# Kernel tuning notes

Measured on AMD Instinct MI355X. Metric: run time of the kernel, lower is better.

Reference implementation:

```python
import jax, jax.numpy as jnp
import numpy as np

EPS = 1e-5

def layer_norm(x, gamma):
    mu = jnp.mean(x, axis=-1, keepdims=True)
    var = jnp.mean(jnp.square(x - mu), axis=-1, keepdims=True)
    return (x - mu) / jnp.sqrt(var + EPS) * gamma

def setup_inputs() -> dict:
    key = jax.random.key(0)
    ks = jax.random.split(key, 10)
    b, n, j = 2, 2048, 2048
    dim, ctx_dim, heads, dim_head, ff_mult = 1024, 1024, 16, 64, 4
    inner = heads * dim_head
    ff_inner = ff_mult * dim
    s = 0.02
    return {
        'x': jax.random.normal(ks[0], (b, n, dim), jnp.float32),
        'context': jax.random.normal(ks[1], (b, j, ctx_dim), jnp.float32),
        'mask': jax.random.randint(ks[2], (b, j), 0, 2, jnp.int32),
        'gamma': jnp.ones((dim,), jnp.float32),
        'ctx_gamma': jnp.ones((ctx_dim,), jnp.float32),
        'Wq': jax.random.normal(ks[3], (dim, inner), jnp.float32) * s,
        'Wkv': jax.random.normal(ks[4], (ctx_dim, 2 * dim_head), jnp.float32) * s,
        'Wout': jax.random.normal(ks[5], (inner, dim), jnp.float32) * s,
        'Wff1': jax.random.normal(ks[6], (dim, 2 * ff_inner), jnp.float32) * s,
        'Wff2': jax.random.normal(ks[7], (ff_inner, dim), jnp.float32) * s,
    }

def reference(x, context, mask, gamma, ctx_gamma, Wq, Wkv, Wout, Wff1, Wff2):
    heads, dim_head = 16, 64
    b, n, dim = x.shape
    scale = dim_head ** -0.5
    xn = layer_norm(x, gamma)                              # [b,n,dim]
    ctx = layer_norm(context, ctx_gamma)                   # [b,j,cd]
    q = (xn @ Wq).reshape(b, n, heads, dim_head).transpose(0, 2, 1, 3) * scale  # [b,h,n,d]
    kv = ctx @ Wkv                                         # [b,j,2d]
    k, v = kv[..., :dim_head], kv[..., dim_head:]          # [b,j,d] each (multi-query)
    sim = jnp.einsum('bhid,bjd->bhij', q, k)               # [b,h,n,j]
    sim = jnp.where((mask == 0)[:, None, None, :], -jnp.inf, sim)
    attn = jax.nn.softmax(sim, axis=-1)
    out = jnp.einsum('bhij,bjd->bhid', attn, v)            # [b,h,n,d]
    out = out.transpose(0, 2, 1, 3).reshape(b, n, heads * dim_head)
    out = out @ Wout                                       # [b,n,dim]
    # parallel SwiGLU FF on normalized x
    h = xn @ Wff1
    ff_inner = Wff2.shape[0]
    a, gate = h[..., :ff_inner], h[..., ff_inner:]
    out = out + (jax.nn.silu(gate) * a) @ Wff2
    return out
```

## Files before the change

### kernel.cpp

```cpp
#include <hip/hip_runtime.h>

typedef unsigned short u16;
typedef unsigned int   u32;
typedef __bf16  bf16x8 __attribute__((ext_vector_type(8)));
typedef __bf16  bf16x2 __attribute__((ext_vector_type(2)));
typedef u16     u16x8  __attribute__((ext_vector_type(8)));
typedef float   f32x4  __attribute__((ext_vector_type(4)));

static __device__ __forceinline__ float b2f(u16 v) {
    return __builtin_bit_cast(float, (u32)(((u32)v) << 16));
}
static __device__ __forceinline__ u16 f2b(float f) {
    u32 u = __builtin_bit_cast(u32, f);
    return (u16)((u + 0x7FFFu + ((u >> 16) & 1u)) >> 16);
}
static __device__ __forceinline__ u32 pack2(float a, float b) {
    bf16x2 t; t[0] = (__bf16)a; t[1] = (__bf16)b;
    return __builtin_bit_cast(u32, t);
}

__global__ __launch_bounds__(256)
void ln_kernel(const float* __restrict__ x, const float* __restrict__ ctx,
               const float* __restrict__ gamma, const float* __restrict__ cgamma,
               u16* __restrict__ xn, u16* __restrict__ ctxn)
{
    const int row = blockIdx.x;
    const int tid = threadIdx.x;
    const float* src; const float* g; u16* dst;
    if (row < 4096) { src = x   + (long)row * 1024;          g = gamma;  dst = xn   + (long)row * 1024; }
    else            { src = ctx + (long)(row - 4096) * 1024; g = cgamma; dst = ctxn + (long)(row - 4096) * 1024; }
    float4 v = ((const float4*)src)[tid];
    float s = v.x + v.y + v.z + v.w;
    float q = v.x*v.x + v.y*v.y + v.z*v.z + v.w*v.w;
#pragma unroll
    for (int off = 32; off; off >>= 1) { s += __shfl_xor(s, off); q += __shfl_xor(q, off); }
    __shared__ float r1[4], r2[4];
    if ((tid & 63) == 0) { r1[tid >> 6] = s; r2[tid >> 6] = q; }
    __syncthreads();
    s = r1[0] + r1[1] + r1[2] + r1[3];
    q = r2[0] + r2[1] + r2[2] + r2[3];
    float mu   = s * (1.0f / 1024.0f);
    float var  = q * (1.0f / 1024.0f) - mu * mu;
    float rstd = rsqrtf(var + 1e-5f);
    float4 gv = ((const float4*)g)[tid];
    ushort4 o;
    o.x = f2b((v.x - mu) * rstd * gv.x);
    o.y = f2b((v.y - mu) * rstd * gv.y);
    o.z = f2b((v.z - mu) * rstd * gv.z);
    o.w = f2b((v.w - mu) * rstd * gv.w);
    ((ushort4*)dst)[tid] = o;
}

__global__ __launch_bounds__(256)
void wconv(const float* __restrict__ W, u16* __restrict__ Wt, int N, int K, float scale)
{
    __shared__ float tile[32][33];
    const int tid = threadIdx.x;
    const int n0 = blockIdx.x * 32;
    const int k0 = blockIdx.y * 32;
    const int r  = tid >> 3;
    const int c4 = (tid & 7) * 4;
    float4 v = *(const float4*)&W[(long)(k0 + r) * N + n0 + c4];
    tile[r][c4 + 0] = v.x; tile[r][c4 + 1] = v.y; tile[r][c4 + 2] = v.z; tile[r][c4 + 3] = v.w;
    __syncthreads();
    ushort4 o;
    o.x = f2b(tile[c4 + 0][r] * scale);
    o.y = f2b(tile[c4 + 1][r] * scale);
    o.z = f2b(tile[c4 + 2][r] * scale);
    o.w = f2b(tile[c4 + 3][r] * scale);
    *(ushort4*)&Wt[(long)(n0 + r) * K + k0 + c4] = o;
}

__global__ __launch_bounds__(256)
void wconv_ff1(const float* __restrict__ W, u16* __restrict__ Wt)
{
    __shared__ float tile[32][33];
    const int tid = threadIdx.x;
    const int a  = blockIdx.x;
    const int k0 = blockIdx.y * 32;
    const int r  = tid >> 3;
    const int c4 = (tid & 7) * 4;
    const int srccol = (c4 < 16) ? (a * 16 + c4) : (4096 + a * 16 + (c4 - 16));
    float4 v = *(const float4*)&W[(long)(k0 + r) * 8192 + srccol];
    tile[r][c4 + 0] = v.x; tile[r][c4 + 1] = v.y; tile[r][c4 + 2] = v.z; tile[r][c4 + 3] = v.w;
    __syncthreads();
    ushort4 o;
    o.x = f2b(tile[c4 + 0][r]);
    o.y = f2b(tile[c4 + 1][r]);
    o.z = f2b(tile[c4 + 2][r]);
    o.w = f2b(tile[c4 + 3][r]);
    *(ushort4*)&Wt[(long)(a * 32 + r) * 1024 + k0 + c4] = o;
}

__global__ __launch_bounds__(256)
void kext_build(const float* __restrict__ kvf, const int* __restrict__ mask,
                u16* __restrict__ kext)
{
    const int gid = blockIdx.x * 256 + threadIdx.x;
    if (gid >= 49152) return;
    const int b = gid / (2048 * 12);
    const int rem = gid - b * (2048 * 12);
    const int j = rem / 12;
    const int c = rem - j * 12;
    u16 ov[8];
    if (c < 8) {
        const float* src = &kvf[((long)b * 2048 + j) * 128 + c * 8];
#pragma unroll
        for (int e = 0; e < 8; ++e) ov[e] = f2b(src[e]);
    } else {
#pragma unroll
        for (int e = 0; e < 8; ++e) ov[e] = 0;
        if (c == 8) ov[0] = mask[b * 2048 + j] ? (u16)0 : f2b(-1e30f);
    }
    uint4 w;
    w.x = (u32)ov[0] | ((u32)ov[1] << 16);
    w.y = (u32)ov[2] | ((u32)ov[3] << 16);
    w.z = (u32)ov[4] | ((u32)ov[5] << 16);
    w.w = (u32)ov[6] | ((u32)ov[7] << 16);
    *(uint4*)&kext[((long)b * 2048 + j) * 96 + c * 8] = w;
}

__global__ __launch_bounds__(256)
void vtrans(const float* __restrict__ kvf, u16* __restrict__ vT)
{
    const int j = blockIdx.x * 256 + threadIdx.x;
    const int d = blockIdx.y;
    const int b = blockIdx.z;
    vT[(long)b * 64 * 2048 + (long)d * 2048 + j] =
        f2b(kvf[((long)b * 2048 + j) * 128 + 64 + d]);
}

#define BM 128
#define BN 128
#define BK 32

template<int EPI>
__global__ __launch_bounds__(256, 2)
void gemm_bt(const u16* __restrict__ A, const u16* __restrict__ Bt,
             void* __restrict__ Cv,
             int K, int lda, int ldb, int ldc,
             long aH, long bH, long cH)
{
    __shared__ __align__(16) u16 sm[2][2][BM * BK];
    const int tid  = threadIdx.x;
    const int wave = tid >> 6;
    const int lane = tid & 63;
    const int tn = blockIdx.x * BN;
    const int tm = blockIdx.y * BM;
    const int z  = blockIdx.z;
    A  += (long)z * aH;
    Bt += (long)z * bH;

    const int arow0 = (tid >> 2);
    const int arow1 = 64 + (tid >> 2);
    const int acs0  = (tid & 3) ^ ((arow0 >> 1) & 3);
    const int acs1  = (tid & 3) ^ ((arow1 >> 1) & 3);
    const int nt = K / BK;

#define STAGE(buf, k0)                                                                              \
    do {                                                                                            \
        __builtin_amdgcn_global_load_lds(                                                           \
            (const __attribute__((address_space(1))) void*)(A + (long)(tm + arow0) * lda + (k0) + acs0 * 8),   \
            (__attribute__((address_space(3))) void*)(&sm[buf][0][(wave * 64) * 8]), 16, 0, 0);     \
        __builtin_amdgcn_global_load_lds(                                                           \
            (const __attribute__((address_space(1))) void*)(A + (long)(tm + arow1) * lda + (k0) + acs1 * 8),   \
            (__attribute__((address_space(3))) void*)(&sm[buf][0][(256 + wave * 64) * 8]), 16, 0, 0); \
        __builtin_amdgcn_global_load_lds(                                                           \
            (const __attribute__((address_space(1))) void*)(Bt + (long)(tn + arow0) * ldb + (k0) + acs0 * 8),  \
            (__attribute__((address_space(3))) void*)(&sm[buf][1][(wave * 64) * 8]), 16, 0, 0);     \
        __builtin_amdgcn_global_load_lds(                                                           \
            (const __attribute__((address_space(1))) void*)(Bt + (long)(tn + arow1) * ldb + (k0) + acs1 * 8),  \
            (__attribute__((address_space(3))) void*)(&sm[buf][1][(256 + wave * 64) * 8]), 16, 0, 0); \
    } while (0)

    STAGE(0, 0);

    f32x4 acc[4][4] = {};
    const int wr   = (wave >> 1) * 64;
    const int wc   = (wave & 1) * 64;
    const int frow = lane & 15;
    const int fk   = lane >> 4;

    for (int t = 0; t < nt; ++t) {
        __syncthreads();
        if (t + 1 < nt) STAGE((t + 1) & 1, (t + 1) * BK);
        const int cur = t & 1;
        bf16x8 af[4], bf[4];
#pragma unroll
        for (int m = 0; m < 4; ++m) {
            int row = wr + m * 16 + frow;
            af[m] = *(const bf16x8*)&sm[cur][0][row * BK + ((fk ^ ((row >> 1) & 3)) * 8)];
        }
#pragma unroll
        for (int n = 0; n < 4; ++n) {
            int row = wc + n * 16 + frow;
            bf[n] = *(const bf16x8*)&sm[cur][1][row * BK + ((fk ^ ((row >> 1) & 3)) * 8)];
        }
#pragma unroll
        for (int m = 0; m < 4; ++m)
#pragma unroll
            for (int n = 0; n < 4; ++n)
                acc[m][n] = __builtin_amdgcn_mfma_f32_16x16x32_bf16(af[m], bf[n], acc[m][n], 0, 0, 0);
    }
#undef STAGE

    const long coff = (long)z * cH;
    if constexpr (EPI == 3) {
#pragma unroll
        for (int m = 0; m < 4; ++m) {
            const int row0 = tm + wr + m * 16 + fk * 4;
#pragma unroll
            for (int np = 0; np < 4; np += 2) {
                const int col = ((tn + wc + np * 16) >> 5) * 16 + frow;
                f32x4 av = acc[m][np], gv = acc[m][np + 1];
#pragma unroll
                for (int r = 0; r < 4; ++r) {
                    const float g = gv[r];
                    const float o = av[r] * g / (1.0f + __expf(-g));
                    ((u16*)Cv)[(long)(row0 + r) * ldc + col] = f2b(o);
                }
            }
        }
    } else {
#pragma unroll
        for (int m = 0; m < 4; ++m) {
            const int row0 = tm + wr + m * 16 + fk * 4;
#pragma unroll
            for (int n = 0; n < 4; ++n) {
                const int col = tn + wc + n * 16 + frow;
#pragma unroll
                for (int r = 0; r < 4; ++r) {
                    const long off = coff + (long)(row0 + r) * ldc + col;
                    const float v = acc[m][n][r];
                    if constexpr (EPI == 0)      ((u16*)Cv)[off] = f2b(v);
                    else if constexpr (EPI == 1) ((float*)Cv)[off] = v;
                    else if constexpr (EPI == 2) ((float*)Cv)[off] += v;
                    else                         atomicAdd(&((float*)Cv)[off], v);
                }
            }
        }
    }
}

__global__ __launch_bounds__(256, 2)
void flash_attn(const u16* __restrict__ qb, const u16* __restrict__ kext,
                const u16* __restrict__ vT, u16* __restrict__ aout)
{
    __shared__ __align__(16) u16 PL[4 * 32 * 128];
    const int tid  = threadIdx.x;
    const int wave = tid >> 6, lane = tid & 63;
    const int frow = lane & 15, fk = lane >> 4;
    const int b = blockIdx.z, h = blockIdx.y;
    const int q0 = blockIdx.x * 128;

    const u16* qbase = qb + ((long)(b * 2048 + q0 + wave * 32)) * 1024 + h * 64;
    bf16x8 bq[2][2];
#pragma unroll
    for (int n = 0; n < 2; ++n)
#pragma unroll
        for (int kk = 0; kk < 2; ++kk)
            bq[n][kk] = *(const bf16x8*)&qbase[(long)(n * 16 + frow) * 1024 + kk * 32 + fk * 8];
    u16x8 tz = {0, 0, 0, 0, 0, 0, 0, 0};
    if (fk == 0) tz[0] = 0x3F80;
    const bf16x8 bqe = __builtin_bit_cast(bf16x8, tz);

    const u16* kbase = kext + (long)b * 2048 * 96;
    const u16* vbase = vT   + (long)b * 64 * 2048;
    u16* plw = &PL[wave * 32 * 128];
    const int swz = frow & 7;

    f32x4 oacc[4][2] = {};
    float mrun[2] = {-1e30f, -1e30f};
    float lrun[2] = {0.0f, 0.0f};

    for (int it = 0; it < 16; ++it) {
        const int j0 = it * 128;
        f32x4 st[8][2] = {};
#pragma unroll
        for (int kk = 0; kk < 3; ++kk) {
            bf16x8 ka[8];
#pragma unroll
            for (int m = 0; m < 8; ++m)
                ka[m] = *(const bf16x8*)&kbase[(long)(j0 + m * 16 + frow) * 96 + kk * 32 + fk * 8];
#pragma unroll
            for (int m = 0; m < 8; ++m) {
                st[m][0] = __builtin_amdgcn_mfma_f32_16x16x32_bf16(ka[m], kk < 2 ? bq[0][kk] : bqe, st[m][0], 0, 0, 0);
                st[m][1] = __builtin_amdgcn_mfma_f32_16x16x32_bf16(ka[m], kk < 2 ? bq[1][kk] : bqe, st[m][1], 0, 0, 0);
            }
        }
        float alpha[2];
#pragma unroll
        for (int n = 0; n < 2; ++n) {
            float pm = st[0][n][0];
#pragma unroll
            for (int m = 0; m < 8; ++m)
#pragma unroll
                for (int r = 0; r < 4; ++r) pm = fmaxf(pm, st[m][n][r]);
            pm = fmaxf(pm, __shfl_xor(pm, 16));
            pm = fmaxf(pm, __shfl_xor(pm, 32));
            const float nm = fmaxf(mrun[n], pm);
            alpha[n] = __expf(mrun[n] - nm);
            mrun[n] = nm;
        }
        float rs[2] = {0.0f, 0.0f};
#pragma unroll
        for (int m = 0; m < 8; ++m) {
            const int j = m * 16 + fk * 4;
            const u32 eladdr = (((j >> 3) ^ swz) * 8) + (j & 7);
#pragma unroll
            for (int n = 0; n < 2; ++n) {
                const float p0 = __expf(st[m][n][0] - mrun[n]);
                const float p1 = __expf(st[m][n][1] - mrun[n]);
                const float p2 = __expf(st[m][n][2] - mrun[n]);
                const float p3 = __expf(st[m][n][3] - mrun[n]);
                rs[n] += (p0 + p1) + (p2 + p3);
                uint2 w; w.x = pack2(p0, p1); w.y = pack2(p2, p3);
                *(uint2*)&plw[(u32)(n * 16 + frow) * 128 + eladdr] = w;
            }
        }
#pragma unroll
        for (int n = 0; n < 2; ++n) {
            rs[n] += __shfl_xor(rs[n], 16);
            rs[n] += __shfl_xor(rs[n], 32);
            lrun[n] = lrun[n] * alpha[n] + rs[n];
        }
#pragma unroll
        for (int mo = 0; mo < 4; ++mo)
#pragma unroll
            for (int no = 0; no < 2; ++no)
#pragma unroll
                for (int r = 0; r < 4; ++r) oacc[mo][no][r] *= alpha[no];
#pragma unroll
        for (int kkv = 0; kkv < 4; ++kkv) {
            bf16x8 va[4], pb[2];
#pragma unroll
            for (int mo = 0; mo < 4; ++mo)
                va[mo] = *(const bf16x8*)&vbase[(long)(mo * 16 + frow) * 2048 + j0 + kkv * 32 + fk * 8];
            const int jj = kkv * 32 + fk * 8;
            const u32 rdoff = ((jj >> 3) ^ swz) * 8;
#pragma unroll
            for (int no = 0; no < 2; ++no)
                pb[no] = *(const bf16x8*)&plw[(u32)(no * 16 + frow) * 128 + rdoff];
#pragma unroll
            for (int mo = 0; mo < 4; ++mo)
#pragma unroll
                for (int no = 0; no < 2; ++no)
                    oacc[mo][no] = __builtin_amdgcn_mfma_f32_16x16x32_bf16(va[mo], pb[no], oacc[mo][no], 0, 0, 0);
        }
    }
#pragma unroll
    for (int no = 0; no < 2; ++no) {
        const float inv = 1.0f / lrun[no];
        const long row = (long)b * 2048 + q0 + wave * 32 + no * 16 + frow;
#pragma unroll
        for (int mo = 0; mo < 4; ++mo) {
            uint2 w;
            w.x = pack2(oacc[mo][no][0] * inv, oacc[mo][no][1] * inv);
            w.y = pack2(oacc[mo][no][2] * inv, oacc[mo][no][3] * inv);
            *(uint2*)&aout[row * 1024 + h * 64 + mo * 16 + fk * 4] = w;
        }
    }
}

extern "C" void kernel_launch(void* const* d_in, const int* in_sizes, int n_in,
                              void* d_out, int out_size, void* d_ws, size_t ws_size,
                              hipStream_t stream)
{
    const float* x      = (const float*)d_in[0];
    const float* ctx    = (const float*)d_in[1];
    const int*   mask   = (const int*)d_in[2];
    const float* gamma  = (const float*)d_in[3];
    const float* cgamma = (const float*)d_in[4];
    const float* Wq     = (const float*)d_in[5];
    const float* Wkv    = (const float*)d_in[6];
    const float* Wout   = (const float*)d_in[7];
    const float* Wff1   = (const float*)d_in[8];
    const float* Wff2   = (const float*)d_in[9];
    float* out = (float*)d_out;

    char* w = (char*)d_ws;
    auto carveB = [&](long bytes) { char* p = w; w += ((bytes + 255) / 256) * 256; return p; };
    u16*   xn     = (u16*)  carveB(4096L * 1024 * 2);
    u16*   ctxn   = (u16*)  carveB(4096L * 1024 * 2);
    u16*   WqT    = (u16*)  carveB(1024L * 1024 * 2);
    u16*   WkvT   = (u16*)  carveB(128L * 1024 * 2);
    u16*   WoutT  = (u16*)  carveB(1024L * 1024 * 2);
    u16*   Wff1Tp = (u16*)  carveB(8192L * 1024 * 2);
    u16*   Wff2T  = (u16*)  carveB(1024L * 4096 * 2);
    u16*   q      = (u16*)  carveB(4096L * 1024 * 2);
    float* kvf    = (float*)carveB(2L * 2048 * 128 * 4);
    u16*   kext   = (u16*)  carveB(2L * 2048 * 96 * 2);
    u16*   vT     = (u16*)  carveB(2L * 64 * 2048 * 2);
    u16*   aout   = (u16*)  carveB(4096L * 1024 * 2);
    u16*   gbuf   = (u16*)  carveB(4096L * 4096 * 2);

    dim3 B(256);

    ln_kernel<<<dim3(8192), B, 0, stream>>>(x, ctx, gamma, cgamma, xn, ctxn);
    wconv<<<dim3(32, 32),  B, 0, stream>>>(Wq,   WqT,   1024, 1024, 0.125f);
    wconv<<<dim3(4, 32),   B, 0, stream>>>(Wkv,  WkvT,  128,  1024, 1.0f);
    wconv<<<dim3(32, 32),  B, 0, stream>>>(Wout, WoutT, 1024, 1024, 1.0f);
    wconv_ff1<<<dim3(256, 32), B, 0, stream>>>(Wff1, Wff1Tp);
    wconv<<<dim3(32, 128), B, 0, stream>>>(Wff2, Wff2T, 1024, 4096, 1.0f);

    gemm_bt<0><<<dim3(8, 32, 1), B, 0, stream>>>(xn, WqT, q, 1024, 1024, 1024, 1024, 0, 0, 0);
    hipMemsetAsync(kvf, 0, 2L * 2048 * 128 * 4, stream);
    gemm_bt<4><<<dim3(1, 32, 4), B, 0, stream>>>(ctxn, WkvT, kvf, 256, 1024, 1024, 128, 256, 256, 0);
    kext_build<<<dim3(192), B, 0, stream>>>(kvf, mask, kext);
    vtrans<<<dim3(8, 64, 2), B, 0, stream>>>(kvf, vT);

    flash_attn<<<dim3(16, 16, 2), B, 0, stream>>>(q, kext, vT, aout);

    gemm_bt<1><<<dim3(8, 32, 1), B, 0, stream>>>(aout, WoutT, out, 1024, 1024, 1024, 1024, 0, 0, 0);
    gemm_bt<3><<<dim3(64, 32, 1), B, 0, stream>>>(xn, Wff1Tp, gbuf, 1024, 1024, 1024, 4096, 0, 0, 0);
    gemm_bt<2><<<dim3(8, 32, 1), B, 0, stream>>>(gbuf, Wff2T, out, 4096, 4096, 4096, 1024, 0, 0, 0);
}
```

Measured before the change: 495.5 us.

## Restructure flash attention with LDS-staged K/V double buffering and separate mask bias

Flash attention now stages K and V tiles into shared memory through async global-to-LDS loads with a swizzled layout and double buffering. It also shrinks the query tile to 64 rows per block, raises the occupancy target, and adds the mask as a float bias instead of an extra MFMA k-step over padded K columns. The goal is to cut redundant global K/V reads and wasted MFMA work, and to overlap loads with compute. Separately, the GEMM remaps workgroup IDs across the 8 XCDs to improve cache locality. The cost is an extra __syncthreads per iteration, more blocks, and LDS pressure.

```diff
diff --git a/kernel.cpp b/kernel.cpp
--- a/kernel.cpp
+++ b/kernel.cpp
@@ -4,7 +4,6 @@
 typedef unsigned int   u32;
 typedef __bf16  bf16x8 __attribute__((ext_vector_type(8)));
 typedef __bf16  bf16x2 __attribute__((ext_vector_type(2)));
-typedef u16     u16x8  __attribute__((ext_vector_type(8)));
 typedef float   f32x4  __attribute__((ext_vector_type(4)));
 
 static __device__ __forceinline__ float b2f(u16 v) {
@@ -94,30 +93,24 @@
 
 __global__ __launch_bounds__(256)
 void kext_build(const float* __restrict__ kvf, const int* __restrict__ mask,
-                u16* __restrict__ kext)
+                u16* __restrict__ kext, float* __restrict__ mbias)
 {
     const int gid = blockIdx.x * 256 + threadIdx.x;
-    if (gid >= 49152) return;
-    const int b = gid / (2048 * 12);
-    const int rem = gid - b * (2048 * 12);
-    const int j = rem / 12;
-    const int c = rem - j * 12;
+    const int b = gid >> 14;
+    const int rem = gid & 16383;
+    const int j = rem >> 3;
+    const int c = rem & 7;
+    const float* src = &kvf[((long)b * 2048 + j) * 128 + c * 8];
     u16 ov[8];
-    if (c < 8) {
-        const float* src = &kvf[((long)b * 2048 + j) * 128 + c * 8];
-#pragma unroll
-        for (int e = 0; e < 8; ++e) ov[e] = f2b(src[e]);
-    } else {
-#pragma unroll
-        for (int e = 0; e < 8; ++e) ov[e] = 0;
-        if (c == 8) ov[0] = mask[b * 2048 + j] ? (u16)0 : f2b(-1e30f);
-    }
+#pragma unroll
+    for (int e = 0; e < 8; ++e) ov[e] = f2b(src[e]);
     uint4 w;
     w.x = (u32)ov[0] | ((u32)ov[1] << 16);
     w.y = (u32)ov[2] | ((u32)ov[3] << 16);
     w.z = (u32)ov[4] | ((u32)ov[5] << 16);
     w.w = (u32)ov[6] | ((u32)ov[7] << 16);
-    *(uint4*)&kext[((long)b * 2048 + j) * 96 + c * 8] = w;
+    *(uint4*)&kext[((long)b * 2048 + j) * 64 + c * 8] = w;
+    if (c == 0) mbias[b * 2048 + j] = mask[b * 2048 + j] ? 0.0f : -1e30f;
 }
 
 __global__ __launch_bounds__(256)
@@ -145,8 +138,13 @@
     const int tid  = threadIdx.x;
     const int wave = tid >> 6;
     const int lane = tid & 63;
-    const int tn = blockIdx.x * BN;
-    const int tm = blockIdx.y * BM;
+    const int gx = gridDim.x;
+    const int nwg = gx * gridDim.y;
+    int wg = blockIdx.y * gx + blockIdx.x;
+    if ((nwg & 7) == 0 && nwg >= 16)
+        wg = (wg & 7) * (nwg >> 3) + (wg >> 3);
+    const int tn = (wg % gx) * BN;
+    const int tm = (wg / gx) * BM;
     const int z  = blockIdx.z;
     A  += (long)z * aH;
     Bt += (long)z * bH;
@@ -242,123 +240,141 @@
     }
 }
 
-__global__ __launch_bounds__(256, 2)
+__global__ __launch_bounds__(256, 4)
 void flash_attn(const u16* __restrict__ qb, const u16* __restrict__ kext,
-                const u16* __restrict__ vT, u16* __restrict__ aout)
-{
-    __shared__ __align__(16) u16 PL[4 * 32 * 128];
+                const u16* __restrict__ vT, const float* __restrict__ mbias,
+                u16* __restrict__ aout)
+{
+    __shared__ __align__(16) u16 Ksm[2][4096];
+    __shared__ __align__(16) u16 Vsm[2][4096];
+    __shared__ __align__(16) u16 Psm[4][1024];
     const int tid  = threadIdx.x;
     const int wave = tid >> 6, lane = tid & 63;
     const int frow = lane & 15, fk = lane >> 4;
     const int b = blockIdx.z, h = blockIdx.y;
-    const int q0 = blockIdx.x * 128;
-
-    const u16* qbase = qb + ((long)(b * 2048 + q0 + wave * 32)) * 1024 + h * 64;
-    bf16x8 bq[2][2];
-#pragma unroll
-    for (int n = 0; n < 2; ++n)
-#pragma unroll
-        for (int kk = 0; kk < 2; ++kk)
-            bq[n][kk] = *(const bf16x8*)&qbase[(long)(n * 16 + frow) * 1024 + kk * 32 + fk * 8];
-    u16x8 tz = {0, 0, 0, 0, 0, 0, 0, 0};
-    if (fk == 0) tz[0] = 0x3F80;
-    const bf16x8 bqe = __builtin_bit_cast(bf16x8, tz);
-
-    const u16* kbase = kext + (long)b * 2048 * 96;
-    const u16* vbase = vT   + (long)b * 64 * 2048;
-    u16* plw = &PL[wave * 32 * 128];
-    const int swz = frow & 7;
-
-    f32x4 oacc[4][2] = {};
-    float mrun[2] = {-1e30f, -1e30f};
-    float lrun[2] = {0.0f, 0.0f};
-
-    for (int it = 0; it < 16; ++it) {
-        const int j0 = it * 128;
-        f32x4 st[8][2] = {};
-#pragma unroll
-        for (int kk = 0; kk < 3; ++kk) {
-            bf16x8 ka[8];
-#pragma unroll
-            for (int m = 0; m < 8; ++m)
-                ka[m] = *(const bf16x8*)&kbase[(long)(j0 + m * 16 + frow) * 96 + kk * 32 + fk * 8];
-#pragma unroll
-            for (int m = 0; m < 8; ++m) {
-                st[m][0] = __builtin_amdgcn_mfma_f32_16x16x32_bf16(ka[m], kk < 2 ? bq[0][kk] : bqe, st[m][0], 0, 0, 0);
-                st[m][1] = __builtin_amdgcn_mfma_f32_16x16x32_bf16(ka[m], kk < 2 ? bq[1][kk] : bqe, st[m][1], 0, 0, 0);
+    const int q0 = blockIdx.x * 64;
+
+    const u16* kx = kext + (long)b * 2048 * 64;
+    const u16* vb = vT   + (long)b * 64 * 2048;
+    const float* mbb = mbias + b * 2048;
+
+    const u16* qbase = qb + ((long)(b * 2048 + q0 + wave * 16 + frow)) * 1024 + h * 64;
+    bf16x8 bq[2];
+#pragma unroll
+    for (int kk = 0; kk < 2; ++kk)
+        bq[kk] = *(const bf16x8*)&qbase[kk * 32 + fk * 8];
+
+#define FSTAGE(buf, j0s)                                                                             \
+    do {                                                                                             \
+        _Pragma("unroll")                                                                            \
+        for (int i = 0; i < 2; ++i) {                                                                \
+            const int slot = i * 256 + tid;                                                          \
+            const int row  = slot >> 3;                                                              \
+            const int csrc = (slot & 7) ^ (row & 7);                                                 \
+            __builtin_amdgcn_global_load_lds(                                                        \
+                (const __attribute__((address_space(1))) void*)(kx + (long)((j0s) + row) * 64 + csrc * 8), \
+                (__attribute__((address_space(3))) void*)(&Ksm[buf][(i * 256 + wave * 64) * 8]), 16, 0, 0); \
+            __builtin_amdgcn_global_load_lds(                                                        \
+                (const __attribute__((address_space(1))) void*)(vb + (long)row * 2048 + (j0s) + csrc * 8),  \
+                (__attribute__((address_space(3))) void*)(&Vsm[buf][(i * 256 + wave * 64) * 8]), 16, 0, 0); \
+        }                                                                                            \
+    } while (0)
+
+    FSTAGE(0, 0);
+
+    f32x4 oacc[4] = {};
+    float mrun = -1e30f, lrun = 0.0f;
+    u16* pw = &Psm[wave][0];
+
+    for (int it = 0; it < 32; ++it) {
+        const int j0 = it * 64;
+        __syncthreads();
+        float4 mb[4];
+#pragma unroll
+        for (int m = 0; m < 4; ++m)
+            mb[m] = *(const float4*)&mbb[j0 + m * 16 + fk * 4];
+        if (it + 1 < 32) FSTAGE((it + 1) & 1, (it + 1) * 64);
+        const int cur = it & 1;
+
+        f32x4 st[4] = {};
+        __builtin_amdgcn_s_setprio(1);
+#pragma unroll
+        for (int kk = 0; kk < 2; ++kk) {
+            bf16x8 ka[4];
+#pragma unroll
+            for (int m = 0; m < 4; ++m) {
+                const int row = m * 16 + frow;
+                ka[m] = *(const bf16x8*)&Ksm[cur][row * 64 + (((kk * 4 + fk) ^ (row & 7)) * 8)];
             }
-        }
-        float alpha[2];
-#pragma unroll
-        for (int n = 0; n < 2; ++n) {
-            float pm = st[0][n][0];
-#pragma unroll
-            for (int m = 0; m < 8; ++m)
-#pragma unroll
-                for (int r = 0; r < 4; ++r) pm = fmaxf(pm, st[m][n][r]);
-            pm = fmaxf(pm, __shfl_xor(pm, 16));
-            pm = fmaxf(pm, __shfl_xor(pm, 32));
-            const float nm = fmaxf(mrun[n], pm);
-            alpha[n] = __expf(mrun[n] - nm);
-            mrun[n] = nm;
-        }
-        float rs[2] = {0.0f, 0.0f};
-#pragma unroll
-        for (int m = 0; m < 8; ++m) {
-            const int j = m * 16 + fk * 4;
-            const u32 eladdr = (((j >> 3) ^ swz) * 8) + (j & 7);
-#pragma unroll
-            for (int n = 0; n < 2; ++n) {
-                const float p0 = __expf(st[m][n][0] - mrun[n]);
-                const float p1 = __expf(st[m][n][1] - mrun[n]);
-                const float p2 = __expf(st[m][n][2] - mrun[n]);
-                const float p3 = __expf(st[m][n][3] - mrun[n]);
-                rs[n] += (p0 + p1) + (p2 + p3);
-                uint2 w; w.x = pack2(p0, p1); w.y = pack2(p2, p3);
-                *(uint2*)&plw[(u32)(n * 16 + frow) * 128 + eladdr] = w;
+#pragma unroll
+            for (int m = 0; m < 4; ++m)
+                st[m] = __builtin_amdgcn_mfma_f32_16x16x32_bf16(ka[m], bq[kk], st[m], 0, 0, 0);
+        }
+        __builtin_amdgcn_s_setprio(0);
+
+        float sb[4][4];
+#pragma unroll
+        for (int m = 0; m < 4; ++m)
+#pragma unroll
+            for (int r = 0; r < 4; ++r) sb[m][r] = st[m][r] + (&mb[m].x)[r];
+        float pm = fmaxf(
+            fmaxf(fmaxf(sb[0][0], sb[0][1]), fmaxf(sb[0][2], sb[0][3])),
+            fmaxf(fmaxf(sb[1][0], sb[1][1]), fmaxf(sb[1][2], sb[1][3])));
+        pm = fmaxf(pm, fmaxf(
+            fmaxf(fmaxf(sb[2][0], sb[2][1]), fmaxf(sb[2][2], sb[2][3])),
+            fmaxf(fmaxf(sb[3][0], sb[3][1]), fmaxf(sb[3][2], sb[3][3]))));
+        pm = fmaxf(pm, __shfl_xor(pm, 16));
+        pm = fmaxf(pm, __shfl_xor(pm, 32));
+        const float nm = fmaxf(mrun, pm);
+        const float alpha = __expf(mrun - nm);
+        mrun = nm;
+
+        float rs = 0.0f;
+#pragma unroll
+        for (int m = 0; m < 4; ++m) {
+            const float p0 = __expf(sb[m][0] - nm);
+            const float p1 = __expf(sb[m][1] - nm);
+            const float p2 = __expf(sb[m][2] - nm);
+            const float p3 = __expf(sb[m][3] - nm);
+            rs += (p0 + p1) + (p2 + p3);
+            const int chunk = (m * 2 + (fk >> 1)) ^ (frow & 7);
+            uint2 w; w.x = pack2(p0, p1); w.y = pack2(p2, p3);
+            *(uint2*)&pw[frow * 64 + chunk * 8 + (fk & 1) * 4] = w;
+        }
+        rs += __shfl_xor(rs, 16);
+        rs += __shfl_xor(rs, 32);
+        lrun = lrun * alpha + rs;
+#pragma unroll
+        for (int mo = 0; mo < 4; ++mo)
+#pragma unroll
+            for (int r = 0; r < 4; ++r) oacc[mo][r] *= alpha;
+
+        __builtin_amdgcn_s_setprio(1);
+#pragma unroll
+        for (int kkv = 0; kkv < 2; ++kkv) {
+            bf16x8 va[4];
+#pragma unroll
+            for (int mo = 0; mo < 4; ++mo) {
+                const int row = mo * 16 + frow;
+                va[mo] = *(const bf16x8*)&Vsm[cur][row * 64 + (((kkv * 4 + fk) ^ (row & 7)) * 8)];
             }
-        }
-#pragma unroll
-        for (int n = 0; n < 2; ++n) {
-            rs[n] += __shfl_xor(rs[n], 16);
-            rs[n] += __shfl_xor(rs[n], 32);
-            lrun[n] = lrun[n] * alpha[n] + rs[n];
-        }
-#pragma unroll
-        for (int mo = 0; mo < 4; ++mo)
-#pragma unroll
-            for (int no = 0; no < 2; ++no)
-#pragma unroll
-                for (int r = 0; r < 4; ++r) oacc[mo][no][r] *= alpha[no];
-#pragma unroll
-        for (int kkv = 0; kkv < 4; ++kkv) {
-            bf16x8 va[4], pb[2];
+            const bf16x8 pb = *(const bf16x8*)&pw[frow * 64 + (((kkv * 4 + fk) ^ (frow & 7)) * 8)];
 #pragma unroll
             for (int mo = 0; mo < 4; ++mo)
-                va[mo] = *(const bf16x8*)&vbase[(long)(mo * 16 + frow) * 2048 + j0 + kkv * 32 + fk * 8];
-            const int jj = kkv * 32 + fk * 8;
-            const u32 rdoff = ((jj >> 3) ^ swz) * 8;
-#pragma unroll
-            for (int no = 0; no < 2; ++no)
-                pb[no] = *(const bf16x8*)&plw[(u32)(no * 16 + frow) * 128 + rdoff];
-#pragma unroll
-            for (int mo = 0; mo < 4; ++mo)
-#pragma unroll
-                for (int no = 0; no < 2; ++no)
-                    oacc[mo][no] = __builtin_amdgcn_mfma_f32_16x16x32_bf16(va[mo], pb[no], oacc[mo][no], 0, 0, 0);
-        }
+                oacc[mo] = __builtin_amdgcn_mfma_f32_16x16x32_bf16(va[mo], pb, oacc[mo], 0, 0, 0);
+        }
+        __builtin_amdgcn_s_setprio(0);
     }
-#pragma unroll
-    for (int no = 0; no < 2; ++no) {
-        const float inv = 1.0f / lrun[no];
-        const long row = (long)b * 2048 + q0 + wave * 32 + no * 16 + frow;
-#pragma unroll
-        for (int mo = 0; mo < 4; ++mo) {
-            uint2 w;
-            w.x = pack2(oacc[mo][no][0] * inv, oacc[mo][no][1] * inv);
-            w.y = pack2(oacc[mo][no][2] * inv, oacc[mo][no][3] * inv);
-            *(uint2*)&aout[row * 1024 + h * 64 + mo * 16 + fk * 4] = w;
-        }
+#undef FSTAGE
+
+    const float inv = 1.0f / lrun;
+    const long row = (long)b * 2048 + q0 + wave * 16 + frow;
+#pragma unroll
+    for (int mo = 0; mo < 4; ++mo) {
+        uint2 w;
+        w.x = pack2(oacc[mo][0] * inv, oacc[mo][1] * inv);
+        w.y = pack2(oacc[mo][2] * inv, oacc[mo][3] * inv);
+        *(uint2*)&aout[row * 1024 + h * 64 + mo * 16 + fk * 4] = w;
     }
 }
 
@@ -389,7 +405,8 @@
     u16*   Wff2T  = (u16*)  carveB(1024L * 4096 * 2);
     u16*   q      = (u16*)  carveB(4096L * 1024 * 2);
     float* kvf    = (float*)carveB(2L * 2048 * 128 * 4);
-    u16*   kext   = (u16*)  carveB(2L * 2048 * 96 * 2);
+    u16*   kext   = (u16*)  carveB(2L * 2048 * 64 * 2);
+    float* mbias  = (float*)carveB(2L * 2048 * 4);
     u16*   vT     = (u16*)  carveB(2L * 64 * 2048 * 2);
     u16*   aout   = (u16*)  carveB(4096L * 1024 * 2);
     u16*   gbuf   = (u16*)  carveB(4096L * 4096 * 2);
@@ -406,10 +423,10 @@
     gemm_bt<0><<<dim3(8, 32, 1), B, 0, stream>>>(xn, WqT, q, 1024, 1024, 1024, 1024, 0, 0, 0);
     hipMemsetAsync(kvf, 0, 2L * 2048 * 128 * 4, stream);
     gemm_bt<4><<<dim3(1, 32, 4), B, 0, stream>>>(ctxn, WkvT, kvf, 256, 1024, 1024, 128, 256, 256, 0);
-    kext_build<<<dim3(192), B, 0, stream>>>(kvf, mask, kext);
+    kext_build<<<dim3(128), B, 0, stream>>>(kvf, mask, kext, mbias);
     vtrans<<<dim3(8, 64, 2), B, 0, stream>>>(kvf, vT);
 
-    flash_attn<<<dim3(16, 16, 2), B, 0, stream>>>(q, kext, vT, aout);
+    flash_attn<<<dim3(32, 16, 2), B, 0, stream>>>(q, kext, vT, mbias, aout);
 
     gemm_bt<1><<<dim3(8, 32, 1), B, 0, stream>>>(aout, WoutT, out, 1024, 1024, 1024, 1024, 0, 0, 0);
     gemm_bt<3><<<dim3(64, 32, 1), B, 0, stream>>>(xn, Wff1Tp, gbuf, 1024, 1024, 1024, 4096, 0, 0, 0);
```

Result: faster. 425.0 us (-14.2%).
